# Kernel optimization log

Hardware: AMD Instinct MI355X
Metric: run time of the kernel (lower is better)

Reference implementation:

```python
import jax, jax.numpy as jnp
import numpy as np

D = 1024
H = 16
HD = D // H
EPS = 1e-6


def setup_inputs() -> dict:
    key = jax.random.key(0)
    ks = jax.random.split(key, 10)
    s = 1.0 / np.sqrt(D)
    inp = {
        "x": jax.random.normal(ks[0], (2, 2048, D), dtype=jnp.float32),
        "Wq": jax.random.uniform(ks[1], (D, D), jnp.float32, -s, s),
        "bq": jax.random.uniform(ks[2], (D,), jnp.float32, -s, s),
        "Wk": jax.random.uniform(ks[3], (D, D), jnp.float32, -s, s),
        "bk": jax.random.uniform(ks[4], (D,), jnp.float32, -s, s),
        "Wv": jax.random.uniform(ks[5], (D, D), jnp.float32, -s, s),
        "bv": jax.random.uniform(ks[6], (D,), jnp.float32, -s, s),
        "Wo": jax.random.uniform(ks[7], (D, D), jnp.float32, -s, s),
        "bo": jax.random.uniform(ks[8], (D,), jnp.float32, -s, s),
        "gamma": jnp.ones((D,), jnp.float32),
        "beta": jnp.zeros((D,), jnp.float32),
    }
    return inp


def _mha(x, Wq, bq, Wk, bk, Wv, bv, Wo, bo, gamma, beta):
    B, S, _ = x.shape
    # Linear projections (torch Linear: x @ W.T + b), split heads -> [B,H,S,hd]
    q = (x @ Wq.T + bq).reshape(B, S, H, HD).transpose(0, 2, 1, 3)
    k = (x @ Wk.T + bk).reshape(B, S, H, HD).transpose(0, 2, 1, 3)
    v = (x @ Wv.T + bv).reshape(B, S, H, HD).transpose(0, 2, 1, 3)
    scores = jnp.einsum("bhqd,bhkd->bhqk", q, k) / jnp.sqrt(jnp.float32(HD))
    attn = jax.nn.softmax(scores, axis=-1)
    ctx = jnp.einsum("bhqk,bhkd->bhqd", attn, v)
    ctx = ctx.transpose(0, 2, 1, 3).reshape(B, S, D)
    out = ctx @ Wo.T + bo  # dropout p=0.0 -> identity
    res = x + out
    mu = jnp.mean(res, axis=-1, keepdims=True)
    var = jnp.mean(jnp.square(res - mu), axis=-1, keepdims=True)
    return (res - mu) / jnp.sqrt(var + EPS) * gamma + beta


def reference(x, Wq, bq, Wk, bk, Wv, bv, Wo, bo, gamma, beta):
    return _mha(x, Wq, bq, Wk, bk, Wv, bv, Wo, bo, gamma, beta)
```

## Files before the change

### kernel.cpp

```cpp
#include <hip/hip_runtime.h>
#include <hip/hip_bf16.h>
#include <math.h>

#define D_MODEL 1024
#define NH 16
#define HDIM 64
#define BB 2
#define SS 2048
#define MTOK (BB*SS)

typedef __hip_bfloat16 bf16;
typedef short s8v __attribute__((ext_vector_type(8)));
typedef float f4v __attribute__((ext_vector_type(4)));
typedef float f16v __attribute__((ext_vector_type(16)));

__device__ __forceinline__ float bf2f(bf16 x) { return __bfloat162float(x); }
__device__ __forceinline__ bf16 f2bf(float x) { return __float2bfloat16(x); }

typedef const __attribute__((address_space(1))) unsigned int* gas_u32;
typedef __attribute__((address_space(3))) unsigned int* las_u32;
#define ASYNC16(gp, lp) __builtin_amdgcn_global_load_lds((gas_u32)(gp), (las_u32)(lp), 16, 0, 0)

#define QSCALE 0.18033688f

__device__ __forceinline__ unsigned int pack_bf16(float a, float b) {
    unsigned int ua = __builtin_bit_cast(unsigned int, a);
    unsigned int ub = __builtin_bit_cast(unsigned int, b);
    return ((ua + 0x8000u) >> 16) | ((ub + 0x8000u) & 0xffff0000u);
}

__global__ __launch_bounds__(256)
void cvt_kernel(const float* __restrict__ x,  const float* __restrict__ wq,
                const float* __restrict__ wk, const float* __restrict__ wv,
                const float* __restrict__ wo, bf16* __restrict__ dst)
{
    const size_t e = ((size_t)blockIdx.x * 256 + threadIdx.x) * 4;
    const size_t M1 = (size_t)1 << 20;
    const float* src; size_t off;
    if      (e < 4 * M1) { src = x;  off = e;          }
    else if (e < 5 * M1) { src = wq; off = e - 4 * M1; }
    else if (e < 6 * M1) { src = wk; off = e - 5 * M1; }
    else if (e < 7 * M1) { src = wv; off = e - 6 * M1; }
    else                 { src = wo; off = e - 7 * M1; }
    const float4 v = *(const float4*)&src[off];
    bf16 h[4] = { f2bf(v.x), f2bf(v.y), f2bf(v.z), f2bf(v.w) };
    *(uint2*)&dst[e] = *(const uint2*)h;
}

__global__ __launch_bounds__(256, 2)
void gemm_qkv(const bf16* __restrict__ X,
              const bf16* __restrict__ Wq, const float* __restrict__ bq,
              const bf16* __restrict__ Wk, const float* __restrict__ bk,
              const bf16* __restrict__ Wv, const float* __restrict__ bv,
              bf16* __restrict__ q_ws, bf16* __restrict__ k_ws, bf16* __restrict__ v_ws)
{
    const int mat = blockIdx.z;
    const bf16*  W    = (mat == 0) ? Wq : ((mat == 1) ? Wk : Wv);
    const float* bias = (mat == 0) ? bq : ((mat == 1) ? bk : bv);

    const int t = threadIdx.x;
    const int lane = t & 63, wave = t >> 6;
    const int wrow = wave >> 1, wcol = wave & 1;
    const int quad = lane >> 4, l15 = lane & 15;

    const bf16 *Ap, *Bp; int m0, n0;
    if (mat < 2) { Ap = X; Bp = W; m0 = blockIdx.y * 128; n0 = blockIdx.x * 128; }
    else         { Ap = W; Bp = X; m0 = blockIdx.x * 128; n0 = blockIdx.y * 128; }

    __shared__ __align__(16) bf16 As[128 * 32];
    __shared__ __align__(16) bf16 Bs[128 * 32];

    f4v acc[4][4];
#pragma unroll
    for (int i = 0; i < 4; i++)
#pragma unroll
        for (int j = 0; j < 4; j++) acc[i][j] = (f4v){0.f, 0.f, 0.f, 0.f};

    const int arow = t >> 2;
    const int acol = (t & 3) * 8;

    for (int kk = 0; kk < D_MODEL; kk += 32) {
        ASYNC16(&Ap[(size_t)(m0 + arow) * D_MODEL + kk + acol],      &As[arow * 32 + acol]);
        ASYNC16(&Ap[(size_t)(m0 + 64 + arow) * D_MODEL + kk + acol], &As[(64 + arow) * 32 + acol]);
        ASYNC16(&Bp[(size_t)(n0 + arow) * D_MODEL + kk + acol],      &Bs[arow * 32 + acol]);
        ASYNC16(&Bp[(size_t)(n0 + 64 + arow) * D_MODEL + kk + acol], &Bs[(64 + arow) * 32 + acol]);
        __syncthreads();

        s8v af[4], bf_[4];
#pragma unroll
        for (int i = 0; i < 4; i++)
            af[i] = *(const s8v*)&As[(wrow * 64 + i * 16 + l15) * 32 + quad * 8];
#pragma unroll
        for (int j = 0; j < 4; j++)
            bf_[j] = *(const s8v*)&Bs[(wcol * 64 + j * 16 + l15) * 32 + quad * 8];
#pragma unroll
        for (int i = 0; i < 4; i++)
#pragma unroll
            for (int j = 0; j < 4; j++)
                acc[i][j] = __builtin_amdgcn_mfma_f32_16x16x32_bf16(af[i], bf_[j], acc[i][j], 0, 0, 0);
        __syncthreads();
    }

    if (mat == 2) {
#pragma unroll
        for (int i = 0; i < 4; i++) {
#pragma unroll
            for (int r = 0; r < 4; r++) {
                const int f = m0 + wrow * 64 + i * 16 + quad * 4 + r;
                const float bv_ = bias[f];
#pragma unroll
                for (int j = 0; j < 4; j++) {
                    const int tok = n0 + wcol * 64 + j * 16 + l15;
                    const int b = tok >> 11, s = tok & 2047;
                    v_ws[((size_t)(b * D_MODEL + f)) * SS + s] = f2bf(acc[i][j][r] + bv_);
                }
            }
        }
    } else {
        bf16* dst = (mat == 0) ? q_ws : k_ws;
        const float scale = (mat == 0) ? QSCALE : 1.0f;
#pragma unroll
        for (int j = 0; j < 4; j++) {
            const int col = n0 + wcol * 64 + j * 16 + l15;
            const float bv_ = bias[col];
            const int h = col >> 6, hd = col & 63;
#pragma unroll
            for (int i = 0; i < 4; i++) {
#pragma unroll
                for (int r = 0; r < 4; r++) {
                    const int row = m0 + wrow * 64 + i * 16 + quad * 4 + r;
                    const int b = row >> 11, s = row & 2047;
                    const float v = (acc[i][j][r] + bv_) * scale;
                    dst[(((size_t)(b * NH + h)) * SS + s) * HDIM + hd] = f2bf(v);
                }
            }
        }
    }
}

__global__ __launch_bounds__(512, 2)
void attn_kernel(const bf16* __restrict__ Q, const bf16* __restrict__ K,
                 const bf16* __restrict__ VtG, bf16* __restrict__ ctx)
{
    const int bh = blockIdx.y;
    const int q0 = blockIdx.x * 256;
    const bf16* Qp = Q   + (size_t)bh * SS * HDIM;
    const bf16* Kp = K   + (size_t)bh * SS * HDIM;
    const bf16* Vp = VtG + (size_t)bh * HDIM * SS;

    __shared__ __align__(16) bf16 Qs[256 * 64];
    __shared__ __align__(16) bf16 Ks[2][128 * 64];
    __shared__ __align__(16) bf16 Vt[2][64 * 128];

    const int t = threadIdx.x;
    const int lane = t & 63, wave = t >> 6;
    const int l31 = lane & 31, L5 = lane >> 5;
    const int qb = wave * 32;

    const int vrow0 = t >> 4,          vcol0 = (t & 15) * 8;
    const int vrow1 = (512 + t) >> 4,  vcol1 = (t & 15) * 8;
    uint4 vv0 = *(const uint4*)&Vp[(size_t)vrow0 * SS + vcol0];
    uint4 vv1 = *(const uint4*)&Vp[(size_t)vrow1 * SS + vcol1];
#pragma unroll
    for (int p = 0; p < 2; p++) {
        const int c = p * 512 + t;
        const int row = c >> 3, j = c & 7;
        ASYNC16(&Kp[(size_t)row * HDIM + (j ^ (row & 7)) * 8], &Ks[0][c * 8]);
    }
#pragma unroll
    for (int p = 0; p < 4; p++) {
        const int c = p * 512 + t;
        const int row = c >> 3, g = (c & 7) ^ (row & 7);
        *(uint4*)&Qs[row * 64 + g * 8] = *(const uint4*)&Qp[(size_t)(q0 + row) * HDIM + (c & 7) * 8];
    }
    {
        union { uint4 u4; uint2 u2[2]; } uu;
        const int cA0 = vcol0,     pA0 = (cA0 & ~12) | ((cA0 & 4) << 1) | ((cA0 & 8) >> 1);
        const int cB0 = vcol0 + 4, pB0 = (cB0 & ~12) | ((cB0 & 4) << 1) | ((cB0 & 8) >> 1);
        uu.u4 = vv0;
        *(uint2*)&Vt[0][vrow0 * 128 + (((pA0 >> 3) ^ (vrow0 & 15)) * 8) + (pA0 & 7)] = uu.u2[0];
        *(uint2*)&Vt[0][vrow0 * 128 + (((pB0 >> 3) ^ (vrow0 & 15)) * 8) + (pB0 & 7)] = uu.u2[1];
        uu.u4 = vv1;
        *(uint2*)&Vt[0][vrow1 * 128 + (((pA0 >> 3) ^ (vrow1 & 15)) * 8) + (pA0 & 7)] = uu.u2[0];
        *(uint2*)&Vt[0][vrow1 * 128 + (((pB0 >> 3) ^ (vrow1 & 15)) * 8) + (pB0 & 7)] = uu.u2[1];
    }
    __syncthreads();

    s8v qf[4];
#pragma unroll
    for (int kc = 0; kc < 4; kc++) {
        const int g = (kc * 2 + L5) ^ (l31 & 7);
        qf[kc] = *(const s8v*)&Qs[(qb + l31) * 64 + g * 8];
    }

    float l_own = 0.f;
    f16v o_acc[2];
#pragma unroll
    for (int i = 0; i < 16; i++) { o_acc[0][i] = 0.f; o_acc[1][i] = 0.f; }

    int cur = 0;
    for (int it = 0; it < SS / 128; ++it) {
        const bool have = (it < SS / 128 - 1);
        const int s0n = (it + 1) * 128;

        uint4 nv0, nv1;
        if (have) {
            nv0 = *(const uint4*)&Vp[(size_t)vrow0 * SS + s0n + vcol0];
            nv1 = *(const uint4*)&Vp[(size_t)vrow1 * SS + s0n + vcol1];
#pragma unroll
            for (int p = 0; p < 2; p++) {
                const int c = p * 512 + t;
                const int row = c >> 3, j = c & 7;
                ASYNC16(&Kp[(size_t)(s0n + row) * HDIM + (j ^ (row & 7)) * 8],
                        &Ks[cur ^ 1][c * 8]);
            }
        }

        const bf16* Ksc = &Ks[cur][0];
        const bf16* Vtc = &Vt[cur][0];
#pragma unroll
        for (int mt = 0; mt < 4; mt++) {
            f16v sc;
#pragma unroll
            for (int i = 0; i < 16; i++) sc[i] = 0.f;
            __builtin_amdgcn_s_setprio(1);
#pragma unroll
            for (int kc = 0; kc < 4; kc++) {
                const int g = (kc * 2 + L5) ^ (l31 & 7);
                const s8v kf = *(const s8v*)&Ksc[(mt * 32 + l31) * 64 + g * 8];
                sc = __builtin_amdgcn_mfma_f32_32x32x16_bf16(kf, qf[kc], sc, 0, 0, 0);
            }
            __builtin_amdgcn_s_setprio(0);
            float tps = 0.f;
#pragma unroll
            for (int i = 0; i < 16; i++) { sc[i] = __builtin_amdgcn_exp2f(sc[i]); tps += sc[i]; }
            l_own += tps;
            unsigned int pk[8];
#pragma unroll
            for (int i = 0; i < 8; i++) pk[i] = pack_bf16(sc[2 * i], sc[2 * i + 1]);
            __builtin_amdgcn_s_setprio(1);
#pragma unroll
            for (int c = 0; c < 2; c++) {
                const s8v pf = *(const s8v*)&pk[c * 4];
#pragma unroll
                for (int dt = 0; dt < 2; dt++) {
                    const int g = (mt * 4 + c * 2 + L5) ^ (l31 & 15);
                    const s8v vf = *(const s8v*)&Vtc[(dt * 32 + l31) * 128 + g * 8];
                    o_acc[dt] = __builtin_amdgcn_mfma_f32_32x32x16_bf16(pf, vf, o_acc[dt], 0, 0, 0);
                }
            }
            __builtin_amdgcn_s_setprio(0);
        }

        if (have) {
            bf16* VtN = &Vt[cur ^ 1][0];
            union { uint4 u4; uint2 u2[2]; } uu;
            const int cA = vcol0,     pA = (cA & ~12) | ((cA & 4) << 1) | ((cA & 8) >> 1);
            const int cB = vcol0 + 4, pB = (cB & ~12) | ((cB & 4) << 1) | ((cB & 8) >> 1);
            uu.u4 = nv0;
            *(uint2*)&VtN[vrow0 * 128 + (((pA >> 3) ^ (vrow0 & 15)) * 8) + (pA & 7)] = uu.u2[0];
            *(uint2*)&VtN[vrow0 * 128 + (((pB >> 3) ^ (vrow0 & 15)) * 8) + (pB & 7)] = uu.u2[1];
            uu.u4 = nv1;
            *(uint2*)&VtN[vrow1 * 128 + (((pA >> 3) ^ (vrow1 & 15)) * 8) + (pA & 7)] = uu.u2[0];
            *(uint2*)&VtN[vrow1 * 128 + (((pB >> 3) ^ (vrow1 & 15)) * 8) + (pB & 7)] = uu.u2[1];
        }
        __syncthreads();
        cur ^= 1;
    }

    const float l_full = l_own + __shfl_xor(l_own, 32);
    const float linv = 1.0f / l_full;
    const int b = bh >> 4, h = bh & 15;
#pragma unroll
    for (int reg = 0; reg < 16; reg++) {
        const int R = (reg & 3) + 8 * (reg >> 2) + 4 * L5;
        const float lr = __shfl(linv, R);
        const int tok = q0 + qb + R;
        const size_t rb = ((size_t)(b * SS + tok)) * D_MODEL + h * 64;
        ctx[rb + l31]      = f2bf(o_acc[0][reg] * lr);
        ctx[rb + 32 + l31] = f2bf(o_acc[1][reg] * lr);
    }
}

__global__ __launch_bounds__(256, 2)
void gemm_oproj(const bf16* __restrict__ Ctx, const bf16* __restrict__ Wo,
                const float* __restrict__ bo, const float* __restrict__ X,
                float* __restrict__ res)
{
    const int m0 = blockIdx.y * 128, n0 = blockIdx.x * 128;
    const int t = threadIdx.x;
    const int lane = t & 63, wave = t >> 6;
    const int wrow = wave >> 1, wcol = wave & 1;
    const int quad = lane >> 4, l15 = lane & 15;

    __shared__ __align__(16) bf16 As[128 * 32];
    __shared__ __align__(16) bf16 Bs[128 * 32];

    f4v acc[4][4];
#pragma unroll
    for (int i = 0; i < 4; i++)
#pragma unroll
        for (int j = 0; j < 4; j++) acc[i][j] = (f4v){0.f, 0.f, 0.f, 0.f};

    const int arow = t >> 2;
    const int acol = (t & 3) * 8;

    for (int kk = 0; kk < D_MODEL; kk += 32) {
        ASYNC16(&Ctx[(size_t)(m0 + arow) * D_MODEL + kk + acol],      &As[arow * 32 + acol]);
        ASYNC16(&Ctx[(size_t)(m0 + 64 + arow) * D_MODEL + kk + acol], &As[(64 + arow) * 32 + acol]);
        ASYNC16(&Wo[(size_t)(n0 + arow) * D_MODEL + kk + acol],       &Bs[arow * 32 + acol]);
        ASYNC16(&Wo[(size_t)(n0 + 64 + arow) * D_MODEL + kk + acol],  &Bs[(64 + arow) * 32 + acol]);
        __syncthreads();

        s8v af[4], bf_[4];
#pragma unroll
        for (int i = 0; i < 4; i++)
            af[i] = *(const s8v*)&As[(wrow * 64 + i * 16 + l15) * 32 + quad * 8];
#pragma unroll
        for (int j = 0; j < 4; j++)
            bf_[j] = *(const s8v*)&Bs[(wcol * 64 + j * 16 + l15) * 32 + quad * 8];
#pragma unroll
        for (int i = 0; i < 4; i++)
#pragma unroll
            for (int j = 0; j < 4; j++)
                acc[i][j] = __builtin_amdgcn_mfma_f32_16x16x32_bf16(af[i], bf_[j], acc[i][j], 0, 0, 0);
        __syncthreads();
    }

#pragma unroll
    for (int j = 0; j < 4; j++) {
        const int col = n0 + wcol * 64 + j * 16 + l15;
        const float bv_ = bo[col];
#pragma unroll
        for (int i = 0; i < 4; i++) {
#pragma unroll
            for (int r = 0; r < 4; r++) {
                const int row = m0 + wrow * 64 + i * 16 + quad * 4 + r;
                const size_t idx = (size_t)row * D_MODEL + col;
                res[idx] = acc[i][j][r] + bv_ + X[idx];
            }
        }
    }
}

__global__ __launch_bounds__(256)
void ln_kernel(const float* __restrict__ res, const float* __restrict__ gamma,
               const float* __restrict__ beta, float* __restrict__ out)
{
    const int row = blockIdx.x;
    const int t = threadIdx.x;
    const float4 v = *(const float4*)&res[(size_t)row * D_MODEL + t * 4];

    float s = v.x + v.y + v.z + v.w;
    float sq = v.x * v.x + v.y * v.y + v.z * v.z + v.w * v.w;
#pragma unroll
    for (int m = 1; m < 64; m <<= 1) {
        s += __shfl_xor(s, m);
        sq += __shfl_xor(sq, m);
    }
    __shared__ float red[8];
    const int wave = t >> 6, lane = t & 63;
    if (lane == 0) { red[wave] = s; red[4 + wave] = sq; }
    __syncthreads();
    s = red[0] + red[1] + red[2] + red[3];
    sq = red[4] + red[5] + red[6] + red[7];
    const float mu = s * (1.0f / D_MODEL);
    const float var = sq * (1.0f / D_MODEL) - mu * mu;
    const float rstd = rsqrtf(var + 1e-6f);

    const float vv[4] = {v.x, v.y, v.z, v.w};
    float4 o;
    o.x = (vv[0] - mu) * rstd * gamma[t * 4 + 0] + beta[t * 4 + 0];
    o.y = (vv[1] - mu) * rstd * gamma[t * 4 + 1] + beta[t * 4 + 1];
    o.z = (vv[2] - mu) * rstd * gamma[t * 4 + 2] + beta[t * 4 + 2];
    o.w = (vv[3] - mu) * rstd * gamma[t * 4 + 3] + beta[t * 4 + 3];
    *(float4*)&out[(size_t)row * D_MODEL + t * 4] = o;
}

extern "C" void kernel_launch(void* const* d_in, const int* in_sizes, int n_in,
                              void* d_out, int out_size, void* d_ws, size_t ws_size,
                              hipStream_t stream) {
    const float* x     = (const float*)d_in[0];
    const float* Wq    = (const float*)d_in[1];
    const float* bq    = (const float*)d_in[2];
    const float* Wk    = (const float*)d_in[3];
    const float* bk    = (const float*)d_in[4];
    const float* Wv    = (const float*)d_in[5];
    const float* bv    = (const float*)d_in[6];
    const float* Wo    = (const float*)d_in[7];
    const float* bo    = (const float*)d_in[8];
    const float* gamma = (const float*)d_in[9];
    const float* beta  = (const float*)d_in[10];
    float* out = (float*)d_out;

    char* ws = (char*)d_ws;
    bf16* xb  = (bf16*)(ws);
    bf16* Wqb = (bf16*)(ws + ((size_t)8 << 20));
    bf16* Wkb = (bf16*)(ws + ((size_t)10 << 20));
    bf16* Wvb = (bf16*)(ws + ((size_t)12 << 20));
    bf16* Wob = (bf16*)(ws + ((size_t)14 << 20));
    bf16*  q_ws   = (bf16*)(ws + ((size_t)16 << 20));
    bf16*  k_ws   = (bf16*)(ws + ((size_t)24 << 20));
    bf16*  v_ws   = (bf16*)(ws + ((size_t)32 << 20));
    bf16*  ctx_ws = (bf16*)(ws + ((size_t)40 << 20));
    float* res_ws = (float*)(ws + ((size_t)16 << 20));

    cvt_kernel<<<8192, 256, 0, stream>>>(x, Wq, Wk, Wv, Wo, xb);
    gemm_qkv<<<dim3(8, 32, 3), 256, 0, stream>>>(xb, Wqb, bq, Wkb, bk, Wvb, bv, q_ws, k_ws, v_ws);
    attn_kernel<<<dim3(8, 32), 512, 0, stream>>>(q_ws, k_ws, v_ws, ctx_ws);
    gemm_oproj<<<dim3(8, 32), 256, 0, stream>>>(ctx_ws, Wob, bo, x, res_ws);
    ln_kernel<<<MTOK, 256, 0, stream>>>(res_ws, gamma, beta, out);
}
```

Baseline: 212.1 us.

## Deepen GEMM K-tiles with swizzled LDS and shrink attention blocks with XCD-aware remap

```diff
diff --git a/kernel.cpp b/kernel.cpp
--- a/kernel.cpp
+++ b/kernel.cpp
@@ -67,8 +67,8 @@
     if (mat < 2) { Ap = X; Bp = W; m0 = blockIdx.y * 128; n0 = blockIdx.x * 128; }
     else         { Ap = W; Bp = X; m0 = blockIdx.x * 128; n0 = blockIdx.y * 128; }
 
-    __shared__ __align__(16) bf16 As[128 * 32];
-    __shared__ __align__(16) bf16 Bs[128 * 32];
+    __shared__ __align__(16) bf16 As[128 * 64];
+    __shared__ __align__(16) bf16 Bs[128 * 64];
 
     f4v acc[4][4];
 #pragma unroll
@@ -76,28 +76,42 @@
 #pragma unroll
         for (int j = 0; j < 4; j++) acc[i][j] = (f4v){0.f, 0.f, 0.f, 0.f};
 
-    const int arow = t >> 2;
-    const int acol = (t & 3) * 8;
-
-    for (int kk = 0; kk < D_MODEL; kk += 32) {
-        ASYNC16(&Ap[(size_t)(m0 + arow) * D_MODEL + kk + acol],      &As[arow * 32 + acol]);
-        ASYNC16(&Ap[(size_t)(m0 + 64 + arow) * D_MODEL + kk + acol], &As[(64 + arow) * 32 + acol]);
-        ASYNC16(&Bp[(size_t)(n0 + arow) * D_MODEL + kk + acol],      &Bs[arow * 32 + acol]);
-        ASYNC16(&Bp[(size_t)(n0 + 64 + arow) * D_MODEL + kk + acol], &Bs[(64 + arow) * 32 + acol]);
+    for (int kk = 0; kk < D_MODEL; kk += 64) {
+#pragma unroll
+        for (int p = 0; p < 4; p++) {
+            const int c = p * 256 + t;
+            const int row = c >> 3, j = c & 7;
+            ASYNC16(&Ap[(size_t)(m0 + row) * D_MODEL + kk + (j ^ (row & 7)) * 8], &As[c * 8]);
+        }
+#pragma unroll
+        for (int p = 0; p < 4; p++) {
+            const int c = p * 256 + t;
+            const int row = c >> 3, j = c & 7;
+            ASYNC16(&Bp[(size_t)(n0 + row) * D_MODEL + kk + (j ^ (row & 7)) * 8], &Bs[c * 8]);
+        }
         __syncthreads();
 
-        s8v af[4], bf_[4];
-#pragma unroll
-        for (int i = 0; i < 4; i++)
-            af[i] = *(const s8v*)&As[(wrow * 64 + i * 16 + l15) * 32 + quad * 8];
-#pragma unroll
-        for (int j = 0; j < 4; j++)
-            bf_[j] = *(const s8v*)&Bs[(wcol * 64 + j * 16 + l15) * 32 + quad * 8];
-#pragma unroll
-        for (int i = 0; i < 4; i++)
-#pragma unroll
-            for (int j = 0; j < 4; j++)
-                acc[i][j] = __builtin_amdgcn_mfma_f32_16x16x32_bf16(af[i], bf_[j], acc[i][j], 0, 0, 0);
+#pragma unroll
+        for (int ks = 0; ks < 2; ks++) {
+            s8v af[4], bf_[4];
+#pragma unroll
+            for (int i = 0; i < 4; i++) {
+                const int row = wrow * 64 + i * 16 + l15;
+                const int g = (ks * 4 + quad) ^ (row & 7);
+                af[i] = *(const s8v*)&As[row * 64 + g * 8];
+            }
+#pragma unroll
+            for (int j = 0; j < 4; j++) {
+                const int row = wcol * 64 + j * 16 + l15;
+                const int g = (ks * 4 + quad) ^ (row & 7);
+                bf_[j] = *(const s8v*)&Bs[row * 64 + g * 8];
+            }
+#pragma unroll
+            for (int i = 0; i < 4; i++)
+#pragma unroll
+                for (int j = 0; j < 4; j++)
+                    acc[i][j] = __builtin_amdgcn_mfma_f32_16x16x32_bf16(af[i], bf_[j], acc[i][j], 0, 0, 0);
+        }
         __syncthreads();
     }
 
@@ -138,17 +152,19 @@
     }
 }
 
-__global__ __launch_bounds__(512, 2)
+__global__ __launch_bounds__(256, 2)
 void attn_kernel(const bf16* __restrict__ Q, const bf16* __restrict__ K,
                  const bf16* __restrict__ VtG, bf16* __restrict__ ctx)
 {
-    const int bh = blockIdx.y;
-    const int q0 = blockIdx.x * 256;
+    const int s_ = blockIdx.x;
+    const int lb = (s_ & 7) * 64 + (s_ >> 3);
+    const int bh = lb >> 4;
+    const int q0 = (lb & 15) * 128;
     const bf16* Qp = Q   + (size_t)bh * SS * HDIM;
     const bf16* Kp = K   + (size_t)bh * SS * HDIM;
     const bf16* Vp = VtG + (size_t)bh * HDIM * SS;
 
-    __shared__ __align__(16) bf16 Qs[256 * 64];
+    __shared__ __align__(16) bf16 Qs[128 * 64];
     __shared__ __align__(16) bf16 Ks[2][128 * 64];
     __shared__ __align__(16) bf16 Vt[2][64 * 128];
 
@@ -157,32 +173,35 @@
     const int l31 = lane & 31, L5 = lane >> 5;
     const int qb = wave * 32;
 
-    const int vrow0 = t >> 4,          vcol0 = (t & 15) * 8;
-    const int vrow1 = (512 + t) >> 4,  vcol1 = (t & 15) * 8;
-    uint4 vv0 = *(const uint4*)&Vp[(size_t)vrow0 * SS + vcol0];
-    uint4 vv1 = *(const uint4*)&Vp[(size_t)vrow1 * SS + vcol1];
-#pragma unroll
-    for (int p = 0; p < 2; p++) {
-        const int c = p * 512 + t;
+    const int vrbase = t >> 4;
+    const int vcol = (t & 15) * 8;
+    uint4 vv[4];
+#pragma unroll
+    for (int p = 0; p < 4; p++)
+        vv[p] = *(const uint4*)&Vp[(size_t)(p * 16 + vrbase) * SS + vcol];
+#pragma unroll
+    for (int p = 0; p < 4; p++) {
+        const int c = p * 256 + t;
         const int row = c >> 3, j = c & 7;
         ASYNC16(&Kp[(size_t)row * HDIM + (j ^ (row & 7)) * 8], &Ks[0][c * 8]);
     }
 #pragma unroll
     for (int p = 0; p < 4; p++) {
-        const int c = p * 512 + t;
+        const int c = p * 256 + t;
         const int row = c >> 3, g = (c & 7) ^ (row & 7);
         *(uint4*)&Qs[row * 64 + g * 8] = *(const uint4*)&Qp[(size_t)(q0 + row) * HDIM + (c & 7) * 8];
     }
+    const int cA = vcol,     pA = (cA & ~12) | ((cA & 4) << 1) | ((cA & 8) >> 1);
+    const int cB = vcol + 4, pB = (cB & ~12) | ((cB & 4) << 1) | ((cB & 8) >> 1);
     {
         union { uint4 u4; uint2 u2[2]; } uu;
-        const int cA0 = vcol0,     pA0 = (cA0 & ~12) | ((cA0 & 4) << 1) | ((cA0 & 8) >> 1);
-        const int cB0 = vcol0 + 4, pB0 = (cB0 & ~12) | ((cB0 & 4) << 1) | ((cB0 & 8) >> 1);
-        uu.u4 = vv0;
-        *(uint2*)&Vt[0][vrow0 * 128 + (((pA0 >> 3) ^ (vrow0 & 15)) * 8) + (pA0 & 7)] = uu.u2[0];
-        *(uint2*)&Vt[0][vrow0 * 128 + (((pB0 >> 3) ^ (vrow0 & 15)) * 8) + (pB0 & 7)] = uu.u2[1];
-        uu.u4 = vv1;
-        *(uint2*)&Vt[0][vrow1 * 128 + (((pA0 >> 3) ^ (vrow1 & 15)) * 8) + (pA0 & 7)] = uu.u2[0];
-        *(uint2*)&Vt[0][vrow1 * 128 + (((pB0 >> 3) ^ (vrow1 & 15)) * 8) + (pB0 & 7)] = uu.u2[1];
+#pragma unroll
+        for (int p = 0; p < 4; p++) {
+            const int vr = p * 16 + vrbase;
+            uu.u4 = vv[p];
+            *(uint2*)&Vt[0][vr * 128 + (((pA >> 3) ^ (vr & 15)) * 8) + (pA & 7)] = uu.u2[0];
+            *(uint2*)&Vt[0][vr * 128 + (((pB >> 3) ^ (vr & 15)) * 8) + (pB & 7)] = uu.u2[1];
+        }
     }
     __syncthreads();
 
@@ -203,13 +222,15 @@
         const bool have = (it < SS / 128 - 1);
         const int s0n = (it + 1) * 128;
 
-        uint4 nv0, nv1;
+        uint4 nv0, nv1, nv2, nv3;
         if (have) {
-            nv0 = *(const uint4*)&Vp[(size_t)vrow0 * SS + s0n + vcol0];
-            nv1 = *(const uint4*)&Vp[(size_t)vrow1 * SS + s0n + vcol1];
-#pragma unroll
-            for (int p = 0; p < 2; p++) {
-                const int c = p * 512 + t;
+            nv0 = *(const uint4*)&Vp[(size_t)(0 * 16 + vrbase) * SS + s0n + vcol];
+            nv1 = *(const uint4*)&Vp[(size_t)(1 * 16 + vrbase) * SS + s0n + vcol];
+            nv2 = *(const uint4*)&Vp[(size_t)(2 * 16 + vrbase) * SS + s0n + vcol];
+            nv3 = *(const uint4*)&Vp[(size_t)(3 * 16 + vrbase) * SS + s0n + vcol];
+#pragma unroll
+            for (int p = 0; p < 4; p++) {
+                const int c = p * 256 + t;
                 const int row = c >> 3, j = c & 7;
                 ASYNC16(&Kp[(size_t)(s0n + row) * HDIM + (j ^ (row & 7)) * 8],
                         &Ks[cur ^ 1][c * 8]);
@@ -255,14 +276,20 @@
         if (have) {
             bf16* VtN = &Vt[cur ^ 1][0];
             union { uint4 u4; uint2 u2[2]; } uu;
-            const int cA = vcol0,     pA = (cA & ~12) | ((cA & 4) << 1) | ((cA & 8) >> 1);
-            const int cB = vcol0 + 4, pB = (cB & ~12) | ((cB & 4) << 1) | ((cB & 8) >> 1);
+            const int vr0 = 0 * 16 + vrbase, vr1 = 1 * 16 + vrbase;
+            const int vr2 = 2 * 16 + vrbase, vr3 = 3 * 16 + vrbase;
             uu.u4 = nv0;
-            *(uint2*)&VtN[vrow0 * 128 + (((pA >> 3) ^ (vrow0 & 15)) * 8) + (pA & 7)] = uu.u2[0];
-            *(uint2*)&VtN[vrow0 * 128 + (((pB >> 3) ^ (vrow0 & 15)) * 8) + (pB & 7)] = uu.u2[1];
+            *(uint2*)&VtN[vr0 * 128 + (((pA >> 3) ^ (vr0 & 15)) * 8) + (pA & 7)] = uu.u2[0];
+            *(uint2*)&VtN[vr0 * 128 + (((pB >> 3) ^ (vr0 & 15)) * 8) + (pB & 7)] = uu.u2[1];
             uu.u4 = nv1;
-            *(uint2*)&VtN[vrow1 * 128 + (((pA >> 3) ^ (vrow1 & 15)) * 8) + (pA & 7)] = uu.u2[0];
-            *(uint2*)&VtN[vrow1 * 128 + (((pB >> 3) ^ (vrow1 & 15)) * 8) + (pB & 7)] = uu.u2[1];
+            *(uint2*)&VtN[vr1 * 128 + (((pA >> 3) ^ (vr1 & 15)) * 8) + (pA & 7)] = uu.u2[0];
+            *(uint2*)&VtN[vr1 * 128 + (((pB >> 3) ^ (vr1 & 15)) * 8) + (pB & 7)] = uu.u2[1];
+            uu.u4 = nv2;
+            *(uint2*)&VtN[vr2 * 128 + (((pA >> 3) ^ (vr2 & 15)) * 8) + (pA & 7)] = uu.u2[0];
+            *(uint2*)&VtN[vr2 * 128 + (((pB >> 3) ^ (vr2 & 15)) * 8) + (pB & 7)] = uu.u2[1];
+            uu.u4 = nv3;
+            *(uint2*)&VtN[vr3 * 128 + (((pA >> 3) ^ (vr3 & 15)) * 8) + (pA & 7)] = uu.u2[0];
+            *(uint2*)&VtN[vr3 * 128 + (((pB >> 3) ^ (vr3 & 15)) * 8) + (pB & 7)] = uu.u2[1];
         }
         __syncthreads();
         cur ^= 1;
@@ -293,8 +320,8 @@
     const int wrow = wave >> 1, wcol = wave & 1;
     const int quad = lane >> 4, l15 = lane & 15;
 
-    __shared__ __align__(16) bf16 As[128 * 32];
-    __shared__ __align__(16) bf16 Bs[128 * 32];
+    __shared__ __align__(16) bf16 As[128 * 64];
+    __shared__ __align__(16) bf16 Bs[128 * 64];
 
     f4v acc[4][4];
 #pragma unroll
@@ -302,28 +329,42 @@
 #pragma unroll
         for (int j = 0; j < 4; j++) acc[i][j] = (f4v){0.f, 0.f, 0.f, 0.f};
 
-    const int arow = t >> 2;
-    const int acol = (t & 3) * 8;
-
-    for (int kk = 0; kk < D_MODEL; kk += 32) {
-        ASYNC16(&Ctx[(size_t)(m0 + arow) * D_MODEL + kk + acol],      &As[arow * 32 + acol]);
-        ASYNC16(&Ctx[(size_t)(m0 + 64 + arow) * D_MODEL + kk + acol], &As[(64 + arow) * 32 + acol]);
-        ASYNC16(&Wo[(size_t)(n0 + arow) * D_MODEL + kk + acol],       &Bs[arow * 32 + acol]);
-        ASYNC16(&Wo[(size_t)(n0 + 64 + arow) * D_MODEL + kk + acol],  &Bs[(64 + arow) * 32 + acol]);
+    for (int kk = 0; kk < D_MODEL; kk += 64) {
+#pragma unroll
+        for (int p = 0; p < 4; p++) {
+            const int c = p * 256 + t;
+            const int row = c >> 3, j = c & 7;
+            ASYNC16(&Ctx[(size_t)(m0 + row) * D_MODEL + kk + (j ^ (row & 7)) * 8], &As[c * 8]);
+        }
+#pragma unroll
+        for (int p = 0; p < 4; p++) {
+            const int c = p * 256 + t;
+            const int row = c >> 3, j = c & 7;
+            ASYNC16(&Wo[(size_t)(n0 + row) * D_MODEL + kk + (j ^ (row & 7)) * 8], &Bs[c * 8]);
+        }
         __syncthreads();
 
-        s8v af[4], bf_[4];
-#pragma unroll
-        for (int i = 0; i < 4; i++)
-            af[i] = *(const s8v*)&As[(wrow * 64 + i * 16 + l15) * 32 + quad * 8];
-#pragma unroll
-        for (int j = 0; j < 4; j++)
-            bf_[j] = *(const s8v*)&Bs[(wcol * 64 + j * 16 + l15) * 32 + quad * 8];
-#pragma unroll
-        for (int i = 0; i < 4; i++)
-#pragma unroll
-            for (int j = 0; j < 4; j++)
-                acc[i][j] = __builtin_amdgcn_mfma_f32_16x16x32_bf16(af[i], bf_[j], acc[i][j], 0, 0, 0);
+#pragma unroll
+        for (int ks = 0; ks < 2; ks++) {
+            s8v af[4], bf_[4];
+#pragma unroll
+            for (int i = 0; i < 4; i++) {
+                const int row = wrow * 64 + i * 16 + l15;
+                const int g = (ks * 4 + quad) ^ (row & 7);
+                af[i] = *(const s8v*)&As[row * 64 + g * 8];
+            }
+#pragma unroll
+            for (int j = 0; j < 4; j++) {
+                const int row = wcol * 64 + j * 16 + l15;
+                const int g = (ks * 4 + quad) ^ (row & 7);
+                bf_[j] = *(const s8v*)&Bs[row * 64 + g * 8];
+            }
+#pragma unroll
+            for (int i = 0; i < 4; i++)
+#pragma unroll
+                for (int j = 0; j < 4; j++)
+                    acc[i][j] = __builtin_amdgcn_mfma_f32_16x16x32_bf16(af[i], bf_[j], acc[i][j], 0, 0, 0);
+        }
         __syncthreads();
     }
 
@@ -407,7 +448,7 @@
 
     cvt_kernel<<<8192, 256, 0, stream>>>(x, Wq, Wk, Wv, Wo, xb);
     gemm_qkv<<<dim3(8, 32, 3), 256, 0, stream>>>(xb, Wqb, bq, Wkb, bk, Wvb, bv, q_ws, k_ws, v_ws);
-    attn_kernel<<<dim3(8, 32), 512, 0, stream>>>(q_ws, k_ws, v_ws, ctx_ws);
+    attn_kernel<<<512, 256, 0, stream>>>(q_ws, k_ws, v_ws, ctx_ws);
     gemm_oproj<<<dim3(8, 32), 256, 0, stream>>>(ctx_ws, Wob, bo, x, res_ws);
     ln_kernel<<<MTOK, 256, 0, stream>>>(res_ws, gamma, beta, out);
 }
```

New measurement: 209.0 us. Within noise of the previous version (-1.4%).
